# Kernel tuning notes

Hardware: AMD Instinct MI355X
Metric: run time of the kernel (lower is better)

Reference implementation:

```python
import jax, jax.numpy as jnp
import numpy as np

N = 30000
E = 480000
D_IN = 128
EPS = 1e-5
NEG_SLOPE = 0.2
# (in_dim, out_channels, heads) per GATConv layer; concat=True everywhere (PyG default)
CFG = [(D_IN, 100, 5), (500, 50, 5), (250, 32, 4), (128, 8, 4), (32, 1, 1)]
BN_DIMS = (500, 250, 128)


def setup_inputs() -> dict:
    key = jax.random.key(0)
    ks = iter(jax.random.split(key, 80))
    inp = {
        "x": jax.random.normal(next(ks), (N, D_IN), jnp.float32),
        "edge_index": jax.random.randint(next(ks), (2, E), 0, N),
        "edge_weight": jax.random.uniform(next(ks), (E, 1), jnp.float32),
    }
    for l, (cin, cout, h) in enumerate(CFG, 1):
        s = 1.0 / np.sqrt(cin)
        inp[f"W{l}"] = jax.random.normal(next(ks), (cin, h * cout), jnp.float32) * s
        inp[f"a_s{l}"] = jax.random.normal(next(ks), (1, h, cout), jnp.float32) * 0.1
        inp[f"a_d{l}"] = jax.random.normal(next(ks), (1, h, cout), jnp.float32) * 0.1
        inp[f"We{l}"] = jax.random.normal(next(ks), (1, h * cout), jnp.float32)
        inp[f"a_e{l}"] = jax.random.normal(next(ks), (1, h, cout), jnp.float32) * 0.1
        inp[f"b{l}"] = jnp.zeros((h * cout,), jnp.float32)
    for l, d in zip((1, 2, 3), BN_DIMS):
        inp[f"g{l}"] = jnp.ones((d,), jnp.float32)
        inp[f"beta{l}"] = jnp.zeros((d,), jnp.float32)
    return inp


def _gat(x, src, dst, ea, W, a_s, a_d, We, a_e, b, heads, cout):
    """PyG GATConv with edge_dim attention (concat=True)."""
    n = x.shape[0]
    h = (x @ W).reshape(n, heads, cout)            # [N,H,C]
    e = (ea @ We).reshape(-1, heads, cout)         # [E,H,C]
    al_src = (h * a_s).sum(-1)                     # [N,H]
    al_dst = (h * a_d).sum(-1)                     # [N,H]
    logit = jax.nn.leaky_relu(al_src[src] + al_dst[dst] + (e * a_e).sum(-1), NEG_SLOPE)
    m = jax.ops.segment_max(logit, dst, num_segments=n)
    m = jnp.where(jnp.isfinite(m), m, 0.0)
    ex = jnp.exp(logit - m[dst])                   # [E,H]
    den = jax.ops.segment_sum(ex, dst, num_segments=n)
    alpha = ex / jnp.maximum(den[dst], 1e-16)      # segment softmax over in-edges of dst
    out = jax.ops.segment_sum(h[src] * alpha[..., None], dst, num_segments=n)
    return out.reshape(n, heads * cout) + b


def _bn(x, g, b):
    mu = x.mean(0)
    var = x.var(0)  # biased, as torch uses for normalization
    return (x - mu) * jax.lax.rsqrt(var + EPS) * g + b


def reference(x, edge_index, edge_weight,
              W1, a_s1, a_d1, We1, a_e1, b1,
              W2, a_s2, a_d2, We2, a_e2, b2,
              W3, a_s3, a_d3, We3, a_e3, b3,
              W4, a_s4, a_d4, We4, a_e4, b4,
              W5, a_s5, a_d5, We5, a_e5, b5,
              g1, beta1, g2, beta2, g3, beta3):
    # add self loops (PyG default) with edge_attr fill_value='mean'
    loop = jnp.arange(N)
    src = jnp.concatenate([edge_index[0], loop])
    dst = jnp.concatenate([edge_index[1], loop])
    ea = jnp.concatenate([edge_weight, jnp.full((N, 1), edge_weight.mean(), edge_weight.dtype)], axis=0)

    h = _gat(x, src, dst, ea, W1, a_s1, a_d1, We1, a_e1, b1, 5, 100)
    h = jax.nn.relu(_bn(h, g1, beta1))
    h = _gat(h, src, dst, ea, W2, a_s2, a_d2, We2, a_e2, b2, 5, 50)
    h = jax.nn.relu(_bn(h, g2, beta2))
    h = _gat(h, src, dst, ea, W3, a_s3, a_d3, We3, a_e3, b3, 4, 32)
    h = jax.nn.relu(_bn(h, g3, beta3))
    h = _gat(h, src, dst, ea, W4, a_s4, a_d4, We4, a_e4, b4, 4, 8)
    h = jax.nn.relu(h)
    h = _gat(h, src, dst, ea, W5, a_s5, a_d5, We5, a_e5, b5, 1, 1)
    return h
```

## Files before the change

### kernel.cpp

```cpp
#include <hip/hip_runtime.h>
#include <hip/hip_bf16.h>
#include <math.h>

#define NN 30000
#define EE 480000
#define ET (EE + NN)
#define NEG_SLOPE 0.2f
#define BN_EPS 1e-5f

struct LayerCfg { int cin, C, H; };
static const LayerCfg g_cfg[5] = {
    {128, 100, 5}, {500, 50, 5}, {250, 32, 4}, {128, 8, 4}, {32, 1, 1}
};

typedef short short8 __attribute__((ext_vector_type(8)));
typedef float f32x4 __attribute__((ext_vector_type(4)));

__device__ __forceinline__ unsigned short f2bf(float f) {
    unsigned int u = __builtin_bit_cast(unsigned int, f);
    u = (u + 0x7FFFu + ((u >> 16) & 1u)) >> 16;
    return (unsigned short)u;
}
__device__ __forceinline__ float bf2f(unsigned short h) {
    unsigned int u = ((unsigned int)h) << 16;
    return __builtin_bit_cast(float, u);
}


struct PrepArgs {
    const float* W[5];
    const float* We[5];
    const float* ae[5];
    unsigned short* bh[5];
    unsigned short* bl[5];
    float* wedot;
    int K[5], N[5], Kp[5], Np[5], C[5], H[5];
};

static const int EBLK = (ET + 255) / 256;

__global__ void prep_fused_kernel(const int* __restrict__ ei, int* __restrict__ rank,
                                  int* __restrict__ cnt, const float* __restrict__ ew,
                                  float* __restrict__ esum, PrepArgs a) {
    __shared__ float sdata[256];
    __shared__ float tile[32][33];
    int b = blockIdx.x;
    int tid = threadIdx.x;

    if (b < EBLK) {
        int e = b * 256 + tid;
        if (e < ET) {
            int d = (e < EE) ? ei[EE + e] : (e - EE);
            rank[e] = atomicAdd(&cnt[d], 1);
        }
        return;
    }
    b -= EBLK;
    if (b < 256) {
        float s = 0.f;
        for (int i = b * 256 + tid; i < EE; i += 65536)
            s += ew[i];
        sdata[tid] = s;
        __syncthreads();
        for (int off = 128; off > 0; off >>= 1) {
            if (tid < off) sdata[tid] += sdata[tid + off];
            __syncthreads();
        }
        if (tid == 0) atomicAdd(esum, sdata[0]);
        return;
    }
    b -= 256;
    int bx = b & 15, by = (b >> 4) & 15, bz = b >> 8;
    int l = bz;
    int tx = tid & 31, ty = tid >> 5;
    if (bx == 0 && by == 0 && ty == 0 && tx < 8) {
        int hd = tx;
        if (hd < a.H[l]) {
            int C = a.C[l];
            const float* We = a.We[l] + hd * C;
            const float* ae = a.ae[l] + hd * C;
            float s = 0.f;
            for (int c = 0; c < C; c++) s += We[c] * ae[c];
            a.wedot[l * 8 + hd] = s;
        }
    }
    int Kp = a.Kp[l], Np = a.Np[l], K = a.K[l], N = a.N[l];
    int kb = bx * 32, nb = by * 32;
    if (kb >= Kp || nb >= Np) return;
    const float* B = a.W[l];
    unsigned short* Bth = a.bh[l];
    unsigned short* Btl = a.bl[l];
#pragma unroll
    for (int i = 0; i < 4; i++) {
        int k = kb + ty + i * 8, n = nb + tx;
        tile[ty + i * 8][tx] = (k < K && n < N) ? B[(size_t)k * N + n] : 0.f;
    }
    __syncthreads();
#pragma unroll
    for (int i = 0; i < 4; i++) {
        int n = nb + ty + i * 8, k = kb + tx;
        if (n < Np && k < Kp) {
            float v = tile[tx][ty + i * 8];
            unsigned short hi = f2bf(v);
            unsigned short lo = f2bf(v - bf2f(hi));
            size_t idx = (size_t)n * Kp + k;
            Bth[idx] = hi;
            Btl[idx] = lo;
        }
    }
}

__global__ void scan_kernel(const int* __restrict__ cnt, int* __restrict__ off) {
    __shared__ int lsum[1024];
    const int T = 1024;
    int t = threadIdx.x;
    int chunk = (NN + T - 1) / T;
    int base = t * chunk;
    int end = min(NN, base + chunk);
    int s = 0;
    for (int i = base; i < end; i++) s += cnt[i];
    lsum[t] = s;
    __syncthreads();
    for (int d = 1; d < T; d <<= 1) {
        int v = (t >= d) ? lsum[t - d] : 0;
        __syncthreads();
        lsum[t] += v;
        __syncthreads();
    }
    int run = (t == 0) ? 0 : lsum[t - 1];
    for (int i = base; i < end; i++) {
        off[i] = run;
        run += cnt[i];
    }
    if (t == 0) off[NN] = ET;
}

__global__ void fill_kernel(const int* __restrict__ ei, const int* __restrict__ rank,
                            const float* __restrict__ ew, const float* __restrict__ esum,
                            const int* __restrict__ off,
                            int* __restrict__ csr_src, float* __restrict__ csr_ea) {
    int e = blockIdx.x * blockDim.x + threadIdx.x;
    if (e >= ET) return;
    int sv, d;
    if (e < EE) { sv = ei[e]; d = ei[EE + e]; }
    else        { sv = e - EE; d = e - EE; }
    int p = off[d] + rank[e];
    csr_src[p] = sv;
    csr_ea[p]  = (e < EE) ? ew[e] : esum[0] * (1.0f / (float)EE);
}

#define GBM 128
#define GBNT 128
#define GBK 32
#define ASTR 36
__global__ __launch_bounds__(256) void gemm_split_kernel(const float* __restrict__ A,
                                                         const unsigned short* __restrict__ Bt_hi,
                                                         const unsigned short* __restrict__ Bt_lo,
                                                         float* __restrict__ Cm,
                                                         unsigned short* __restrict__ Ch16,
                                                         int M, int Kp, int Nc,
                                                         const float* __restrict__ colsum,
                                                         const float* __restrict__ colsumsq,
                                                         const float* __restrict__ g,
                                                         const float* __restrict__ beta,
                                                         int D) {
    __shared__ short AsH[GBM * ASTR];
    __shared__ short AsL[GBM * ASTR];
    __shared__ short BsH[GBNT * ASTR];
    __shared__ short BsL[GBNT * ASTR];
    __shared__ float sscale[512];
    __shared__ float sshift[512];
    int tid = threadIdx.x;
    bool bn = (colsum != nullptr);
    if (bn) {
        for (int c = tid; c < Kp; c += 256) {
            float sc = 0.f, sh = 0.f;
            if (c < D) {
                float mu = colsum[c] * (1.0f / (float)NN);
                float var = colsumsq[c] * (1.0f / (float)NN) - mu * mu;
                sc = g[c] * rsqrtf(var + BN_EPS);
                sh = beta[c] - mu * sc;
            }
            sscale[c] = sc;
            sshift[c] = sh;
        }
        __syncthreads();
    }
    int wave = tid >> 6, lane = tid & 63;
    int q = lane >> 4, r = lane & 15;
    int m0 = blockIdx.y * GBM, n0 = blockIdx.x * GBNT;
    int wm = (wave & 1) * 64, wn = (wave >> 1) * 64;
    f32x4 acc[4][4];
#pragma unroll
    for (int i = 0; i < 4; i++)
#pragma unroll
        for (int j = 0; j < 4; j++) acc[i][j] = (f32x4)(0.f);

    int arow2 = tid >> 1;
    int acol2 = (tid & 1) * 16;
    int brow = tid >> 2;
    int bcol = (tid & 3) * 8;

    int ksteps = Kp / GBK;
    for (int ks = 0; ks < ksteps; ks++) {
        int k0 = ks * GBK;
        {
            int m = m0 + arow2;
            float v[16];
            if (m < M) {
                const float* Ap = A + (size_t)m * Kp + k0 + acol2;
                float4 f0 = *(const float4*)(Ap);
                float4 f1 = *(const float4*)(Ap + 4);
                float4 f2 = *(const float4*)(Ap + 8);
                float4 f3 = *(const float4*)(Ap + 12);
                v[0]=f0.x; v[1]=f0.y; v[2]=f0.z; v[3]=f0.w;
                v[4]=f1.x; v[5]=f1.y; v[6]=f1.z; v[7]=f1.w;
                v[8]=f2.x; v[9]=f2.y; v[10]=f2.z; v[11]=f2.w;
                v[12]=f3.x; v[13]=f3.y; v[14]=f3.z; v[15]=f3.w;
                if (bn) {
                    int cb = k0 + acol2;
#pragma unroll
                    for (int i = 0; i < 16; i++)
                        v[i] = fmaxf(v[i] * sscale[cb + i] + sshift[cb + i], 0.f);
                }
            } else {
#pragma unroll
                for (int i = 0; i < 16; i++) v[i] = 0.f;
            }
#pragma unroll
            for (int i = 0; i < 16; i++) {
                unsigned short hi = f2bf(v[i]);
                unsigned short lo = f2bf(v[i] - bf2f(hi));
                AsH[arow2 * ASTR + acol2 + i] = (short)hi;
                AsL[arow2 * ASTR + acol2 + i] = (short)lo;
            }
        }
#pragma unroll
        for (int p = 0; p < 2; p++) {
            int row = p * 64 + brow;
            size_t gidx = (size_t)(n0 + row) * Kp + k0 + bcol;
            *((uint4*)(BsH + row * ASTR + bcol)) = *((const uint4*)(Bt_hi + gidx));
            *((uint4*)(BsL + row * ASTR + bcol)) = *((const uint4*)(Bt_lo + gidx));
        }
        __syncthreads();
        short8 ah[4], al[4], bh[4], bl[4];
#pragma unroll
        for (int i = 0; i < 4; i++) {
            ah[i] = *((const short8*)(AsH + (wm + i * 16 + r) * ASTR + q * 8));
            al[i] = *((const short8*)(AsL + (wm + i * 16 + r) * ASTR + q * 8));
        }
#pragma unroll
        for (int j = 0; j < 4; j++) {
            bh[j] = *((const short8*)(BsH + (wn + j * 16 + r) * ASTR + q * 8));
            bl[j] = *((const short8*)(BsL + (wn + j * 16 + r) * ASTR + q * 8));
        }
#pragma unroll
        for (int i = 0; i < 4; i++)
#pragma unroll
            for (int j = 0; j < 4; j++) {
                acc[i][j] = __builtin_amdgcn_mfma_f32_16x16x32_bf16(ah[i], bh[j], acc[i][j], 0, 0, 0);
                acc[i][j] = __builtin_amdgcn_mfma_f32_16x16x32_bf16(ah[i], bl[j], acc[i][j], 0, 0, 0);
                acc[i][j] = __builtin_amdgcn_mfma_f32_16x16x32_bf16(al[i], bh[j], acc[i][j], 0, 0, 0);
            }
        __syncthreads();
    }
#pragma unroll
    for (int i = 0; i < 4; i++) {
#pragma unroll
        for (int j = 0; j < 4; j++) {
#pragma unroll
            for (int reg = 0; reg < 4; reg++) {
                int mrow = m0 + wm + i * 16 + q * 4 + reg;
                int ncol = n0 + wn + j * 16 + r;
                if (mrow < M && ncol < Nc) {
                    float val = acc[i][j][reg];
                    if (Cm)   Cm[(size_t)mrow * Nc + ncol] = val;
                    if (Ch16) Ch16[(size_t)mrow * Nc + ncol] = f2bf(val);
                }
            }
        }
    }
}

__global__ void gemv_l5_kernel(const float* __restrict__ X, const float* __restrict__ W,
                               const float* __restrict__ a_s, const float* __restrict__ a_d,
                               float* __restrict__ h, float* __restrict__ al_src,
                               float* __restrict__ al_dst) {
    __shared__ float w[32];
    if (threadIdx.x < 32) w[threadIdx.x] = W[threadIdx.x];
    __syncthreads();
    int n = blockIdx.x * blockDim.x + threadIdx.x;
    if (n >= NN) return;
    const float* row = X + (size_t)n * 32;
    float s = 0.f;
#pragma unroll
    for (int i = 0; i < 8; i++) {
        float4 f = *(const float4*)(row + i * 4);
        s += f.x * w[i * 4] + f.y * w[i * 4 + 1] + f.z * w[i * 4 + 2] + f.w * w[i * 4 + 3];
    }
    h[n] = s;
    al_src[n] = s * a_s[0];
    al_dst[n] = s * a_d[0];
}

__global__ void al_wave_h16_kernel(const unsigned short* __restrict__ h16,
                                   const float* __restrict__ a_s,
                                   const float* __restrict__ a_d,
                                   float* __restrict__ al_src, float* __restrict__ al_dst,
                                   int H, int C, int HCp) {
    int w = (blockIdx.x * blockDim.x + threadIdx.x) >> 6;
    int lane = threadIdx.x & 63;
    if (w >= NN) return;
    const unsigned short* row = h16 + (size_t)w * HCp;
    float s1[5] = {0.f, 0.f, 0.f, 0.f, 0.f};
    float s2[5] = {0.f, 0.f, 0.f, 0.f, 0.f};
#pragma unroll
    for (int hd = 0; hd < 5; hd++) {
        if (hd >= H) break;
        int base = hd * C;
        for (int c = lane * 2; c < C; c += 128) {
            unsigned int u = *(const unsigned int*)(row + base + c);
            float v0 = bf2f((unsigned short)(u & 0xffffu));
            float v1 = bf2f((unsigned short)(u >> 16));
            s1[hd] += v0 * a_s[base + c] + v1 * a_s[base + c + 1];
            s2[hd] += v0 * a_d[base + c] + v1 * a_d[base + c + 1];
        }
    }
#pragma unroll
    for (int hd = 0; hd < 5; hd++) {
        if (hd >= H) break;
#pragma unroll
        for (int off = 32; off > 0; off >>= 1) {
            s1[hd] += __shfl_xor(s1[hd], off, 64);
            s2[hd] += __shfl_xor(s2[hd], off, 64);
        }
    }
    if (lane == 0) {
#pragma unroll
        for (int hd = 0; hd < 5; hd++) {
            if (hd >= H) break;
            al_src[(size_t)w * H + hd] = s1[hd];
            al_dst[(size_t)w * H + hd] = s2[hd];
        }
    }
}

__global__ void attn_kernel(const float* __restrict__ al_src,
                            const float* __restrict__ al_dst,
                            const int* __restrict__ csr_src,
                            const float* __restrict__ csr_ea,
                            const float* __restrict__ we_dot,
                            const int* __restrict__ off,
                            float* __restrict__ alpha_t,
                            float* __restrict__ inv_den, int H, int PH, int NH) {
    int t = blockIdx.x * blockDim.x + threadIdx.x;
    if (t >= NH) return;
    int n = t / H, hd = t - n * H;
    int s = off[n], e = off[n + 1];
    float ad = al_dst[(size_t)n * H + hd];
    float wd = we_dot[hd];
    float* arow = alpha_t + hd;
    float den = 0.f;
    int p = s;
    for (; p + 3 < e; p += 4) {
        int s0 = csr_src[p], s1 = csr_src[p + 1], s2 = csr_src[p + 2], s3 = csr_src[p + 3];
        float w0 = csr_ea[p], w1 = csr_ea[p + 1], w2 = csr_ea[p + 2], w3 = csr_ea[p + 3];
        float l0 = al_src[(size_t)s0 * H + hd] + ad + w0 * wd;
        float l1 = al_src[(size_t)s1 * H + hd] + ad + w1 * wd;
        float l2 = al_src[(size_t)s2 * H + hd] + ad + w2 * wd;
        float l3 = al_src[(size_t)s3 * H + hd] + ad + w3 * wd;
        l0 = (l0 >= 0.f) ? l0 : NEG_SLOPE * l0;
        l1 = (l1 >= 0.f) ? l1 : NEG_SLOPE * l1;
        l2 = (l2 >= 0.f) ? l2 : NEG_SLOPE * l2;
        l3 = (l3 >= 0.f) ? l3 : NEG_SLOPE * l3;
        float e0 = __expf(l0), e1 = __expf(l1), e2 = __expf(l2), e3 = __expf(l3);
        arow[(size_t)p * PH] = e0;
        arow[(size_t)(p + 1) * PH] = e1;
        arow[(size_t)(p + 2) * PH] = e2;
        arow[(size_t)(p + 3) * PH] = e3;
        den += e0 + e1 + e2 + e3;
    }
    for (; p < e; p++) {
        float lg = al_src[(size_t)csr_src[p] * H + hd] + ad + csr_ea[p] * wd;
        lg = (lg >= 0.f) ? lg : NEG_SLOPE * lg;
        float ex = __expf(lg);
        arow[(size_t)p * PH] = ex;
        den += ex;
    }
    inv_den[t] = 1.f / fmaxf(den, 1e-16f);
}

#define AGG_T 64
#define IDX_STR 68
#define AL_ROW 68
__global__ void aggregate_slab_lds_kernel(const unsigned short* __restrict__ h16,
                                          const float* __restrict__ alpha_t,
                                          const int* __restrict__ off,
                                          const int* __restrict__ csr_src,
                                          const float* __restrict__ bias,
                                          const float* __restrict__ inv_den,
                                          float* __restrict__ out,
                                          int C, int H, int PH, int HC, int hp,
                                          int lns, int lcps, int npr, int nhs,
                                          int algstr, int tight, int relu, int opitch) {
    extern __shared__ char smem[];
    int cps = 1 << lcps;
    int G = 256 >> lcps;
    int* sidx = (int*)smem;
    float* sal = (float*)(smem + (size_t)G * IDX_STR * 4);
    __shared__ int s_maxt;

    int vs = blockIdx.x & 7;
    int nb = blockIdx.x >> 3;
    int slab = vs & ((1 << lns) - 1);
    int rep  = vs >> lns;
    int tid = threadIdx.x;
    int lc = tid & (cps - 1);
    int g = tid >> lcps;
    int nl = nb * G + g;
    bool active = (nl < npr);
    int n = rep * npr + (active ? nl : 0);

    int slab_j = slab << (lcps + 2);
    int j = slab_j + (lc << 2);
    int hlo = slab_j / C;
    int hhi = (slab_j + (cps << 2) - 1) / C;
    if (hhi > H - 1) hhi = H - 1;
    int nval = hhi - hlo + 1;

    int hdA = j / C;
    int hdB = (j + 3) / C;
    int bnd = (hdA + 1) * C - j;
    bnd = (bnd > 4) ? 4 : bnd;
    int selA = hdA - hlo; if (selA >= nhs) selA = nhs - 1;
    int selB = hdB - hlo; if (selB >= nhs) selB = nhs - 1;
    int hA = (hdA < H) ? hdA : H - 1;
    int hB = (hdB < H) ? hdB : H - 1;

    int s = active ? off[n] : 0;
    int e = active ? off[n + 1] : 0;
    int nt = (e - s + AGG_T - 1) / AGG_T;

    if (tid == 0) s_maxt = 0;
    __syncthreads();
    if (lc == 0 && active && nt > 0) atomicMax(&s_maxt, nt);
    __syncthreads();
    int maxt = s_maxt;

    int hpb = hp << 1;
    const char* hb = (const char*)(h16 + j);
    int* myidx = sidx + g * IDX_STR;
    float* myal = sal + (size_t)g * algstr;
    float ac0 = 0.f, ac1 = 0.f, ac2 = 0.f, ac3 = 0.f;

    for (int t = 0; t < maxt; t++) {
        int base = s + t * AGG_T;
        int cnt = e - base;
        if (cnt < 0) cnt = 0;
        if (cnt > AGG_T) cnt = AGG_T;
        __syncthreads();
        for (int q = lc; q < cnt; q += cps)
            myidx[q] = csr_src[base + q] * hpb;
        for (int r = 0; r < nhs; r++) {
            bool hv = (r < nval);
            const float* ar = alpha_t + hlo + r;
            float* dst = myal + r * AL_ROW;
            for (int q = lc; q < cnt; q += cps)
                dst[q] = hv ? ar[(size_t)(base + q) * PH] : 0.f;
        }
        __syncthreads();
        if (tight) {
            const float* aA = myal + selA * AL_ROW;
            int q = 0;
            for (; q + 3 < cnt; q += 4) {
                int b0 = myidx[q], b1 = myidx[q + 1], b2 = myidx[q + 2], b3 = myidx[q + 3];
                float a0 = aA[q], a1 = aA[q + 1], a2 = aA[q + 2], a3 = aA[q + 3];
                ushort4 u0 = *(const ushort4*)(hb + b0);
                ushort4 u1 = *(const ushort4*)(hb + b1);
                ushort4 u2 = *(const ushort4*)(hb + b2);
                ushort4 u3 = *(const ushort4*)(hb + b3);
                ac0 += a0 * bf2f(u0.x); ac1 += a0 * bf2f(u0.y);
                ac2 += a0 * bf2f(u0.z); ac3 += a0 * bf2f(u0.w);
                ac0 += a1 * bf2f(u1.x); ac1 += a1 * bf2f(u1.y);
                ac2 += a1 * bf2f(u1.z); ac3 += a1 * bf2f(u1.w);
                ac0 += a2 * bf2f(u2.x); ac1 += a2 * bf2f(u2.y);
                ac2 += a2 * bf2f(u2.z); ac3 += a2 * bf2f(u2.w);
                ac0 += a3 * bf2f(u3.x); ac1 += a3 * bf2f(u3.y);
                ac2 += a3 * bf2f(u3.z); ac3 += a3 * bf2f(u3.w);
            }
            for (; q < cnt; q++) {
                int b0 = myidx[q];
                float a0 = aA[q];
                ushort4 uv = *(const ushort4*)(hb + b0);
                ac0 += a0 * bf2f(uv.x); ac1 += a0 * bf2f(uv.y);
                ac2 += a0 * bf2f(uv.z); ac3 += a0 * bf2f(uv.w);
            }
        } else {
            const float* aA = myal + selA * AL_ROW;
            const float* aB = myal + selB * AL_ROW;
            int q = 0;
            for (; q + 3 < cnt; q += 4) {
                int b0 = myidx[q], b1 = myidx[q + 1], b2 = myidx[q + 2], b3 = myidx[q + 3];
                float a0 = aA[q], a1 = aA[q + 1], a2 = aA[q + 2], a3 = aA[q + 3];
                float c0 = aB[q], c1 = aB[q + 1], c2 = aB[q + 2], c3 = aB[q + 3];
                ushort4 u0 = *(const ushort4*)(hb + b0);
                ushort4 u1 = *(const ushort4*)(hb + b1);
                ushort4 u2 = *(const ushort4*)(hb + b2);
                ushort4 u3 = *(const ushort4*)(hb + b3);
                ac0 += ((0 < bnd) ? a0 : c0) * bf2f(u0.x);
                ac1 += ((1 < bnd) ? a0 : c0) * bf2f(u0.y);
                ac2 += ((2 < bnd) ? a0 : c0) * bf2f(u0.z);
                ac3 += ((3 < bnd) ? a0 : c0) * bf2f(u0.w);
                ac0 += ((0 < bnd) ? a1 : c1) * bf2f(u1.x);
                ac1 += ((1 < bnd) ? a1 : c1) * bf2f(u1.y);
                ac2 += ((2 < bnd) ? a1 : c1) * bf2f(u1.z);
                ac3 += ((3 < bnd) ? a1 : c1) * bf2f(u1.w);
                ac0 += ((0 < bnd) ? a2 : c2) * bf2f(u2.x);
                ac1 += ((1 < bnd) ? a2 : c2) * bf2f(u2.y);
                ac2 += ((2 < bnd) ? a2 : c2) * bf2f(u2.z);
                ac3 += ((3 < bnd) ? a2 : c2) * bf2f(u2.w);
                ac0 += ((0 < bnd) ? a3 : c3) * bf2f(u3.x);
                ac1 += ((1 < bnd) ? a3 : c3) * bf2f(u3.y);
                ac2 += ((2 < bnd) ? a3 : c3) * bf2f(u3.z);
                ac3 += ((3 < bnd) ? a3 : c3) * bf2f(u3.w);
            }
            for (; q < cnt; q++) {
                int b0 = myidx[q];
                float a0 = aA[q], c0 = aB[q];
                ushort4 uv = *(const ushort4*)(hb + b0);
                ac0 += ((0 < bnd) ? a0 : c0) * bf2f(uv.x);
                ac1 += ((1 < bnd) ? a0 : c0) * bf2f(uv.y);
                ac2 += ((2 < bnd) ? a0 : c0) * bf2f(uv.z);
                ac3 += ((3 < bnd) ? a0 : c0) * bf2f(uv.w);
            }
        }
    }
    if (!active) return;
    float invA = inv_den[(size_t)n * H + hA];
    float invB = inv_den[(size_t)n * H + hB];
    float o0 = ac0 * ((0 < bnd) ? invA : invB) + ((j + 0 < HC) ? bias[j + 0] : 0.f);
    float o1 = ac1 * ((1 < bnd) ? invA : invB) + ((j + 1 < HC) ? bias[j + 1] : 0.f);
    float o2 = ac2 * ((2 < bnd) ? invA : invB) + ((j + 2 < HC) ? bias[j + 2] : 0.f);
    float o3 = ac3 * ((3 < bnd) ? invA : invB) + ((j + 3 < HC) ? bias[j + 3] : 0.f);
    if (relu) {
        o0 = fmaxf(o0, 0.f); o1 = fmaxf(o1, 0.f);
        o2 = fmaxf(o2, 0.f); o3 = fmaxf(o3, 0.f);
    }
    *(float4*)(out + (size_t)n * opitch + j) = make_float4(o0, o1, o2, o3);
}

__global__ void aggregate_kernel(const float* __restrict__ hfeat,
                                 const float* __restrict__ alpha_t,
                                 const int* __restrict__ off, const int* __restrict__ csr_src,
                                 const float* __restrict__ bias,
                                 const float* __restrict__ inv_den,
                                 float* __restrict__ out, int total) {
    int t = blockIdx.x * blockDim.x + threadIdx.x;
    if (t >= total) return;
    int n = t;
    int s = off[n], e = off[n + 1];
    float acc = 0.f;
    int p = s;
    for (; p + 3 < e; p += 4) {
        acc += alpha_t[p] * hfeat[csr_src[p]]
             + alpha_t[p + 1] * hfeat[csr_src[p + 1]]
             + alpha_t[p + 2] * hfeat[csr_src[p + 2]]
             + alpha_t[p + 3] * hfeat[csr_src[p + 3]];
    }
    for (; p < e; p++) acc += alpha_t[p] * hfeat[csr_src[p]];
    out[n] = acc * inv_den[n] + bias[0];
}


__global__ void bn_stats_kernel(const float* __restrict__ x, float* __restrict__ colsum,
                                float* __restrict__ colsumsq, int D, int pitch) {
    int rows_per_block = (NN + gridDim.x - 1) / gridDim.x;
    int r0 = blockIdx.x * rows_per_block;
    int r1 = min(NN, r0 + rows_per_block);
    int c0 = threadIdx.x;
    int c1 = threadIdx.x + 256;
    float s0 = 0.f, q0 = 0.f, s1 = 0.f, q1 = 0.f;
    for (int r = r0; r < r1; r++) {
        const float* row = x + (size_t)r * pitch;
        if (c0 < D) { float v = row[c0]; s0 += v; q0 += v * v; }
        if (c1 < D) { float v = row[c1]; s1 += v; q1 += v * v; }
    }
    if (c0 < D) { atomicAdd(&colsum[c0], s0); atomicAdd(&colsumsq[c0], q0); }
    if (c1 < D) { atomicAdd(&colsum[c1], s1); atomicAdd(&colsumsq[c1], q1); }
}


static inline size_t align_up(size_t v, size_t a) { return (v + a - 1) / a * a; }

extern "C" void kernel_launch(void* const* d_in, const int* in_sizes, int n_in,
                              void* d_out, int out_size, void* d_ws, size_t ws_size,
                              hipStream_t stream) {
    const float* x_in = (const float*)d_in[0];
    const int* ei     = (const int*)d_in[1];
    const float* ew   = (const float*)d_in[2];

    char* pws = (char*)d_ws;
    size_t off_b = 0;
    auto alloc = [&](size_t bytes) -> void* {
        void* rp = pws + off_b;
        off_b = align_up(off_b + bytes, 256);
        return rp;
    };
    float* B0      = (float*)alloc((size_t)NN * 4);
    float* B1      = (float*)alloc((size_t)NN * 512 * 4);
    unsigned short* H16 = (unsigned short*)alloc((size_t)NN * 512 * 2);
    float* alpha_t = (float*)alloc((size_t)ET * 5 * 4);
    unsigned short* Wt_hi = (unsigned short*)alloc((size_t)600 * 512 * 2);
    unsigned short* Wt_lo = (unsigned short*)alloc((size_t)600 * 512 * 2);
    float* al_src  = (float*)alloc((size_t)NN * 5 * 4);
    float* al_dst  = (float*)alloc((size_t)NN * 5 * 4);
    float* inv_den = (float*)alloc((size_t)NN * 5 * 4);
    float* csr_ea  = (float*)alloc((size_t)ET * 4);
    int* rankb     = (int*)alloc((size_t)ET * 4);
    int* csr_src   = (int*)alloc((size_t)ET * 4);
    int* offarr    = (int*)alloc((size_t)(NN + 1) * 4);
    float* we_dot  = (float*)alloc(40 * 4);
    float* esum    = (float*)alloc(4);
    int* cnt       = (int*)alloc((size_t)NN * 4);
    float* colsum_all   = (float*)alloc(3 * 512 * 4);
    float* colsumsq_all = (float*)alloc(3 * 512 * 4);
    char* zero_end = pws + off_b;
    (void)ws_size; (void)n_in; (void)in_sizes; (void)out_size;

    int Kp[5], Np[5], hp[5];
    size_t wtoff[5];
    size_t acc_off = 0;
    for (int l = 0; l < 5; l++) {
        int K = g_cfg[l].cin, HC = g_cfg[l].C * g_cfg[l].H;
        Kp[l] = (K + 31) / 32 * 32;
        Np[l] = (HC + 127) / 128 * 128;
        hp[l] = (HC >= 64) ? ((HC + 63) / 64 * 64) : ((HC + 7) / 8 * 8);
        wtoff[l] = acc_off;
        acc_off += (size_t)Kp[l] * Np[l];
    }

    PrepArgs pa;
    for (int l = 0; l < 5; l++) {
        pa.W[l]  = (const float*)d_in[3 + l * 6 + 0];
        pa.We[l] = (const float*)d_in[3 + l * 6 + 3];
        pa.ae[l] = (const float*)d_in[3 + l * 6 + 4];
        pa.bh[l] = Wt_hi + wtoff[l];
        pa.bl[l] = Wt_lo + wtoff[l];
        pa.K[l] = g_cfg[l].cin;
        pa.N[l] = g_cfg[l].C * g_cfg[l].H;
        pa.Kp[l] = Kp[l];
        pa.Np[l] = Np[l];
        pa.C[l] = g_cfg[l].C;
        pa.H[l] = g_cfg[l].H;
    }
    pa.wedot = we_dot;

    hipMemsetAsync(esum, 0, (size_t)(zero_end - (char*)esum), stream);
    int ebl = EBLK;
    prep_fused_kernel<<<ebl + 256 + 1280, 256, 0, stream>>>(ei, rankb, cnt, ew, esum, pa);
    scan_kernel<<<1, 1024, 0, stream>>>(cnt, offarr);
    fill_kernel<<<ebl, 256, 0, stream>>>(ei, rankb, ew, esum, offarr, csr_src, csr_ea);

    for (int l = 0; l < 5; l++) {
        const LayerCfg& cf = g_cfg[l];
        int H = cf.H, C = cf.C;
        int HC = H * C;
        int PH = H;
        const float* a_s = (const float*)d_in[3 + l * 6 + 1];
        const float* a_d = (const float*)d_in[3 + l * 6 + 2];
        const float* b   = (const float*)d_in[3 + l * 6 + 5];

        const float* X = (l == 0) ? x_in : B1;
        float* outbuf = (l == 4) ? (float*)d_out : B1;
        int opitch = (l == 4) ? 1 : Kp[l + 1];
        int NH = NN * H;
        int alblocks = (NN * 64 + 255) / 256;

        if (l == 4) {
            gemv_l5_kernel<<<(NN + 255) / 256, 256, 0, stream>>>(
                X, pa.W[4], a_s, a_d, B0, al_src, al_dst);
        } else {
            const float* cs = (l >= 1) ? colsum_all + (l - 1) * 512 : nullptr;
            const float* cq = (l >= 1) ? colsumsq_all + (l - 1) * 512 : nullptr;
            const float* gg = (l >= 1) ? (const float*)d_in[33 + (l - 1) * 2 + 0] : nullptr;
            const float* bb = (l >= 1) ? (const float*)d_in[33 + (l - 1) * 2 + 1] : nullptr;
            int Din = (l >= 1) ? g_cfg[l - 1].C * g_cfg[l - 1].H : 0;
            dim3 ggrid(Np[l] / GBNT, (NN + GBM - 1) / GBM);
            gemm_split_kernel<<<ggrid, 256, 0, stream>>>(X, Wt_hi + wtoff[l], Wt_lo + wtoff[l],
                                                         nullptr, H16,
                                                         NN, Kp[l], hp[l], cs, cq, gg, bb, Din);
            al_wave_h16_kernel<<<alblocks, 256, 0, stream>>>(H16, a_s, a_d, al_src, al_dst, H, C, hp[l]);
        }

        attn_kernel<<<(NH + 255) / 256, 256, 0, stream>>>(al_src, al_dst, csr_src, csr_ea,
                                                          we_dot + l * 8, offarr, alpha_t,
                                                          inv_den, H, PH, NH);

        if (l == 4) {
            aggregate_kernel<<<(NN + 255) / 256, 256, 0, stream>>>(
                B0, alpha_t, offarr, csr_src, b, inv_den, outbuf, NN);
        } else {
            int cps = (hp[l] >= 64) ? 16 : 8;
            int lcps = (cps == 16) ? 4 : 3;
            int slabcols = cps * 4;
            int nslabs = hp[l] / slabcols;
            int lns = (nslabs == 8) ? 3 : (nslabs == 4) ? 2 : (nslabs == 2) ? 1 : 0;
            int dup = 8 / nslabs;
            int npr = NN / dup;
            int G = 256 / cps;
            int gx = 8 * ((npr + G - 1) / G);
            int nhs = 1;
            for (int sbi = 0; sbi < nslabs; sbi++) {
                int j0 = sbi * slabcols;
                int span = (j0 + slabcols - 1) / C - j0 / C + 1;
                if (span > nhs) nhs = span;
            }
            int algstr = nhs * AL_ROW + 4;
            int tight = ((C & 3) == 0) ? 1 : 0;
            size_t smem = (size_t)G * IDX_STR * 4 + (size_t)G * algstr * 4;
            aggregate_slab_lds_kernel<<<gx, 256, smem, stream>>>(
                H16, alpha_t, offarr, csr_src, b, inv_den, outbuf,
                C, H, PH, HC, hp[l], lns, lcps, npr, nhs, algstr, tight,
                (l == 3) ? 1 : 0, opitch);
        }

        if (l < 3) {
            bn_stats_kernel<<<512, 256, 0, stream>>>(outbuf, colsum_all + l * 512,
                                                     colsumsq_all + l * 512, HC, opitch);
        }
    }
}
```

Measured before the change: 743.0 us.

## Sort nodes by in-degree and process attention/aggregation in degree-binned order

Builds a degree histogram, scans it and scatters node ids into a degree-sorted permutation. The attention and aggregation kernels then map threads to nodes through this permutation, so neighbouring lanes handle nodes with similar edge counts. The aim is to cut wave divergence and load imbalance from uneven per-node loop lengths. In exchange it adds three small kernels and an extra indirection. It also scatters writes to inv_den and outputs, which loses the sequential locality of node-ordered access.

```diff
diff --git a/kernel.cpp b/kernel.cpp
--- a/kernel.cpp
+++ b/kernel.cpp
@@ -7,6 +7,7 @@
 #define ET (EE + NN)
 #define NEG_SLOPE 0.2f
 #define BN_EPS 1e-5f
+#define NBIN 512
 
 struct LayerCfg { int cin, C, H; };
 static const LayerCfg g_cfg[5] = {
@@ -147,6 +148,44 @@
     int p = off[d] + rank[e];
     csr_src[p] = sv;
     csr_ea[p]  = (e < EE) ? ew[e] : esum[0] * (1.0f / (float)EE);
+}
+
+
+__global__ void deghist_kernel(const int* __restrict__ cnt, int* __restrict__ hist) {
+    __shared__ int lh[NBIN];
+    int tid = threadIdx.x;
+    lh[tid] = 0; lh[tid + 256] = 0;
+    __syncthreads();
+    for (int n = blockIdx.x * 256 + tid; n < NN; n += gridDim.x * 256) {
+        int d = cnt[n]; if (d > NBIN - 1) d = NBIN - 1;
+        atomicAdd(&lh[d], 1);
+    }
+    __syncthreads();
+    if (lh[tid]) atomicAdd(&hist[tid], lh[tid]);
+    if (lh[tid + 256]) atomicAdd(&hist[tid + 256], lh[tid + 256]);
+}
+
+__global__ void binscan_kernel(const int* __restrict__ hist, int* __restrict__ binoff) {
+    __shared__ int l[NBIN];
+    int t = threadIdx.x;
+    l[t] = hist[t];
+    __syncthreads();
+    for (int d = 1; d < NBIN; d <<= 1) {
+        int v = (t >= d) ? l[t - d] : 0;
+        __syncthreads();
+        l[t] += v;
+        __syncthreads();
+    }
+    binoff[t] = l[t] - hist[t];
+}
+
+__global__ void degscatter_kernel(const int* __restrict__ cnt, const int* __restrict__ binoff,
+                                  int* __restrict__ cursor, int* __restrict__ perm) {
+    int n = blockIdx.x * 256 + threadIdx.x;
+    if (n >= NN) return;
+    int d = cnt[n]; if (d > NBIN - 1) d = NBIN - 1;
+    int pos = binoff[d] + atomicAdd(&cursor[d], 1);
+    perm[pos] = n;
 }
 
 #define GBM 128
@@ -351,11 +390,13 @@
                             const float* __restrict__ csr_ea,
                             const float* __restrict__ we_dot,
                             const int* __restrict__ off,
+                            const int* __restrict__ perm,
                             float* __restrict__ alpha_t,
                             float* __restrict__ inv_den, int H, int PH, int NH) {
     int t = blockIdx.x * blockDim.x + threadIdx.x;
     if (t >= NH) return;
-    int n = t / H, hd = t - n * H;
+    int slot = t / H, hd = t - slot * H;
+    int n = perm[slot];
     int s = off[n], e = off[n + 1];
     float ad = al_dst[(size_t)n * H + hd];
     float wd = we_dot[hd];
@@ -387,7 +428,7 @@
         arow[(size_t)p * PH] = ex;
         den += ex;
     }
-    inv_den[t] = 1.f / fmaxf(den, 1e-16f);
+    inv_den[(size_t)n * H + hd] = 1.f / fmaxf(den, 1e-16f);
 }
 
 #define AGG_T 64
@@ -399,6 +440,7 @@
                                           const int* __restrict__ csr_src,
                                           const float* __restrict__ bias,
                                           const float* __restrict__ inv_den,
+                                          const int* __restrict__ perm,
                                           float* __restrict__ out,
                                           int C, int H, int PH, int HC, int hp,
                                           int lns, int lcps, int npr, int nhs,
@@ -419,7 +461,7 @@
     int g = tid >> lcps;
     int nl = nb * G + g;
     bool active = (nl < npr);
-    int n = rep * npr + (active ? nl : 0);
+    int n = perm[rep * npr + (active ? nl : 0)];
 
     int slab_j = slab << (lcps + 2);
     int j = slab_j + (lc << 2);
@@ -554,10 +596,11 @@
                                  const int* __restrict__ off, const int* __restrict__ csr_src,
                                  const float* __restrict__ bias,
                                  const float* __restrict__ inv_den,
+                                 const int* __restrict__ perm,
                                  float* __restrict__ out, int total) {
     int t = blockIdx.x * blockDim.x + threadIdx.x;
     if (t >= total) return;
-    int n = t;
+    int n = perm[t];
     int s = off[n], e = off[n + 1];
     float acc = 0.f;
     int p = s;
@@ -619,9 +662,13 @@
     int* rankb     = (int*)alloc((size_t)ET * 4);
     int* csr_src   = (int*)alloc((size_t)ET * 4);
     int* offarr    = (int*)alloc((size_t)(NN + 1) * 4);
+    int* perm      = (int*)alloc((size_t)NN * 4);
+    int* binoff    = (int*)alloc((size_t)NBIN * 4);
     float* we_dot  = (float*)alloc(40 * 4);
     float* esum    = (float*)alloc(4);
     int* cnt       = (int*)alloc((size_t)NN * 4);
+    int* hist      = (int*)alloc((size_t)NBIN * 4);
+    int* cursor    = (int*)alloc((size_t)NBIN * 4);
     float* colsum_all   = (float*)alloc(3 * 512 * 4);
     float* colsumsq_all = (float*)alloc(3 * 512 * 4);
     char* zero_end = pws + off_b;
@@ -660,6 +707,9 @@
     prep_fused_kernel<<<ebl + 256 + 1280, 256, 0, stream>>>(ei, rankb, cnt, ew, esum, pa);
     scan_kernel<<<1, 1024, 0, stream>>>(cnt, offarr);
     fill_kernel<<<ebl, 256, 0, stream>>>(ei, rankb, ew, esum, offarr, csr_src, csr_ea);
+    deghist_kernel<<<64, 256, 0, stream>>>(cnt, hist);
+    binscan_kernel<<<1, NBIN, 0, stream>>>(hist, binoff);
+    degscatter_kernel<<<(NN + 255) / 256, 256, 0, stream>>>(cnt, binoff, cursor, perm);
 
     for (int l = 0; l < 5; l++) {
         const LayerCfg& cf = g_cfg[l];
@@ -693,12 +743,12 @@
         }
 
         attn_kernel<<<(NH + 255) / 256, 256, 0, stream>>>(al_src, al_dst, csr_src, csr_ea,
-                                                          we_dot + l * 8, offarr, alpha_t,
+                                                          we_dot + l * 8, offarr, perm, alpha_t,
                                                           inv_den, H, PH, NH);
 
         if (l == 4) {
             aggregate_kernel<<<(NN + 255) / 256, 256, 0, stream>>>(
-                B0, alpha_t, offarr, csr_src, b, inv_den, outbuf, NN);
+                B0, alpha_t, offarr, csr_src, b, inv_den, perm, outbuf, NN);
         } else {
             int cps = (hp[l] >= 64) ? 16 : 8;
             int lcps = (cps == 16) ? 4 : 3;
@@ -719,7 +769,7 @@
             int tight = ((C & 3) == 0) ? 1 : 0;
             size_t smem = (size_t)G * IDX_STR * 4 + (size_t)G * algstr * 4;
             aggregate_slab_lds_kernel<<<gx, 256, smem, stream>>>(
-                H16, alpha_t, offarr, csr_src, b, inv_den, outbuf,
+                H16, alpha_t, offarr, csr_src, b, inv_den, perm, outbuf,
                 C, H, PH, HC, hp[l], lns, lcps, npr, nhs, algstr, tight,
                 (l == 3) ? 1 : 0, opitch);
         }
```

After: 867.7 us. 16.8% more time.
